# Kernel optimization log

Hardware: AMD Instinct MI355X
Metric: run time of the kernel (lower is better)

## Reference

```python
import jax, jax.numpy as jnp
import numpy as np

BATCH = 4        # opt.batch_size
NPATCH = 4096    # patches per batch element
DIM = 256        # feature dim
MAXC = 5         # self.max_classes
T = 0.07         # opt.nce_T
NEG_FILL = -10.0


def setup_inputs() -> dict:
    key = jax.random.key(0)
    k1, k2, k3 = jax.random.split(key, 3)
    N = BATCH * NPATCH
    features_src = jax.random.normal(k1, (N, DIM), jnp.float32)
    features_tgt = jax.random.normal(k2, (N, DIM), jnp.float32)
    classes = jax.random.randint(k3, (N,), 0, MAXC, dtype=jnp.int32)
    return {"features_src": features_src, "features_tgt": features_tgt, "classes": classes}


def reference(features_src, features_tgt, classes):
    # feat_k = feat_k.detach()
    tgt = jax.lax.stop_gradient(features_tgt)

    # positive logits: per-row dot product, divided by temperature
    pos = jnp.sum(features_src * tgt, axis=-1) / T            # [N]

    src_b = features_src.reshape(BATCH, NPATCH, DIM)
    tgt_b = tgt.reshape(BATCH, NPATCH, DIM)
    cls = classes.reshape(BATCH, NPATCH)

    # full negative logit matrix per batch element
    logits = jnp.einsum('bnd,bmd->bnm', src_b, tgt_b)         # [B, n, n]
    same = cls[:, :, None] == cls[:, None, :]                 # [B, n, n] same-class mask

    # per-class smallest negative logit: min over (row in class c, col not in class c)
    row_min = jnp.min(jnp.where(same, jnp.inf, logits), axis=2)          # [B, n]
    class_eq = cls[:, :, None] == jnp.arange(MAXC)[None, None, :]        # [B, n, C]
    class_min = jnp.min(jnp.where(class_eq, row_min[:, :, None], jnp.inf), axis=1)  # [B, C]
    smallest = jnp.minimum(class_min, NEG_FILL) / T                      # [B, C]
    counts = jnp.sum(class_eq, axis=1)                                   # [B, C]

    # per-row pad value and pad multiplicity (num_pairs_should - num_pairs_is = count_c - 1)
    sm_row = jnp.take_along_axis(smallest, cls, axis=1)                  # [B, n]
    npad = jnp.take_along_axis(counts, cls, axis=1) - 1                  # [B, n]

    # logsumexp over [pos, negatives (other classes only), npad copies of smallest]
    lse_neg = jax.nn.logsumexp(jnp.where(same, -jnp.inf, logits / T), axis=2)  # [B, n]
    pad_term = jnp.where(npad > 0,
                         jnp.log(jnp.maximum(npad, 1).astype(jnp.float32)) + sm_row,
                         -jnp.inf)
    pos_b = pos.reshape(BATCH, NPATCH)
    lse = jax.nn.logsumexp(jnp.stack([pos_b, lse_neg, pad_term], axis=-1), axis=-1)
    loss = lse - pos_b                                                   # CE with label 0

    # match torch ordering: rows concatenated per batch, grouped by class (stable)
    order = jnp.argsort(cls, axis=1)  # jnp.argsort is stable
    return jnp.take_along_axis(loss, order, axis=1).reshape(-1)
```

## Files before the change

kernel.cpp:

```cpp
#include <hip/hip_runtime.h>
#include <cstdint>

#define NBATCH 4
#define NPATCH 4096
#define MAXC   5
#define NCHUNK 8
#define RBLOCKS 16
#define GRID_MAIN (NBATCH * RBLOCKS * NCHUNK)
#define SCALE  14.285714285714286f
#define SCALE2 20.609929006188747f
#define LN2F   0.6931471805599453f
#define NEGH  -1.0e38f
#define NEGFILL_T -142.85714285714286f
#define NROWS (NBATCH * NPATCH)

typedef __attribute__((ext_vector_type(8))) short short8;
typedef __attribute__((ext_vector_type(4))) float f32x4;
typedef __attribute__((ext_vector_type(4))) unsigned int u32x4;

__device__ __forceinline__ float fexp2(float x) { return __builtin_amdgcn_exp2f(x); }
__device__ __forceinline__ float flog2(float x) { return __builtin_amdgcn_logf(x); }

__device__ __forceinline__ unsigned short f2bf(float f) {
  uint32_t u = __builtin_bit_cast(uint32_t, f);
  u = (u + 0x7FFFu + ((u >> 16) & 1u)) >> 16;
  return (unsigned short)u;
}

__device__ __forceinline__ void glds16(const void* g, void* l) {
  __builtin_amdgcn_global_load_lds(
      (const __attribute__((address_space(1))) uint32_t*)g,
      (__attribute__((address_space(3))) uint32_t*)l, 16, 0, 0);
}


__global__ __launch_bounds__(256) void k_aux(const float* __restrict__ src,
                                             const float* __restrict__ tgt,
                                             const int* __restrict__ classes,
                                             unsigned short* __restrict__ tgtb,
                                             unsigned short* __restrict__ srcb,
                                             float* __restrict__ pos,
                                             int* __restrict__ outpos,
                                             int* __restrict__ counts) {
  int blk = blockIdx.x;
  if (blk < 512) {
    __shared__ uint4 sS[2][544], sT[2][544];
    int t    = threadIdx.x;
    int half = t >> 7;
    int tt   = t & 127;
    int tl   = blk * 2 + half;
    int row16 = tt >> 3;
    int kg    = tt & 7;
    size_t rowbase = (size_t)(tl * 16 + row16) * 256 + kg * 32;
    const float4* rs  = (const float4*)(src + rowbase);
    const float4* rt_ = (const float4*)(tgt + rowbase);
    float d = 0.f;
#pragma unroll
    for (int jj = 0; jj < 4; ++jj) {
      float4 sa = rs[jj * 2], sb = rs[jj * 2 + 1];
      float4 ta = rt_[jj * 2], tb = rt_[jj * 2 + 1];
      d += sa.x * ta.x + sa.y * ta.y + sa.z * ta.z + sa.w * ta.w
         + sb.x * tb.x + sb.y * tb.y + sb.z * tb.z + sb.w * tb.w;
      union { ushort4 h[2]; uint4 u; } pk;
      int li = (kg * 4 + jj) * 17 + row16;
      pk.h[0].x = f2bf(sa.x * SCALE2); pk.h[0].y = f2bf(sa.y * SCALE2);
      pk.h[0].z = f2bf(sa.z * SCALE2); pk.h[0].w = f2bf(sa.w * SCALE2);
      pk.h[1].x = f2bf(sb.x * SCALE2); pk.h[1].y = f2bf(sb.y * SCALE2);
      pk.h[1].z = f2bf(sb.z * SCALE2); pk.h[1].w = f2bf(sb.w * SCALE2);
      sS[half][li] = pk.u;
      pk.h[0].x = f2bf(ta.x); pk.h[0].y = f2bf(ta.y);
      pk.h[0].z = f2bf(ta.z); pk.h[0].w = f2bf(ta.w);
      pk.h[1].x = f2bf(tb.x); pk.h[1].y = f2bf(tb.y);
      pk.h[1].z = f2bf(tb.z); pk.h[1].w = f2bf(tb.w);
      sT[half][li] = pk.u;
    }
    d += __shfl_xor(d, 1, 64);
    d += __shfl_xor(d, 2, 64);
    d += __shfl_xor(d, 4, 64);
    if (kg == 0) pos[tl * 16 + row16] = d * SCALE;

    __syncthreads();
    uint4* osrc = (uint4*)srcb + (size_t)tl * 512;
    uint4* otgt = (uint4*)tgtb + (size_t)tl * 512;
#pragma unroll
    for (int c = 0; c < 4; ++c) {
      int g  = c * 128 + tt;
      int li = (g >> 4) * 17 + (g & 15);
      osrc[g] = sS[half][li];
      otgt[g] = sT[half][li];
    }
    return;
  }

  __shared__ int sa[MAXC * 256];
  __shared__ int sb2[MAXC * 256];
  int b = blk - 512, t = threadIdx.x;
  int base = b * NPATCH + t * 16;
  int cv[16];
#pragma unroll
  for (int e = 0; e < 16; ++e) cv[e] = classes[base + e];
  int cnt[MAXC];
#pragma unroll
  for (int c = 0; c < MAXC; ++c) {
    cnt[c] = 0;
#pragma unroll
    for (int e = 0; e < 16; ++e)
      if (cv[e] == c) cnt[c]++;
  }
#pragma unroll
  for (int c = 0; c < MAXC; ++c) sa[c * 256 + t] = cnt[c];
  __syncthreads();

  int* rp = sa; int* wp = sb2;
  for (int d = 1; d < 256; d <<= 1) {
#pragma unroll
    for (int c = 0; c < MAXC; ++c) {
      int v = rp[c * 256 + t];
      if (t >= d) v += rp[c * 256 + t - d];
      wp[c * 256 + t] = v;
    }
    __syncthreads();
    int* tmp = rp; rp = wp; wp = tmp;
  }

  int tot[MAXC], excl[MAXC], off[MAXC + 1];
  off[0] = 0;
#pragma unroll
  for (int c = 0; c < MAXC; ++c) {
    tot[c]  = rp[c * 256 + 255];
    excl[c] = rp[c * 256 + t] - cnt[c];
    off[c + 1] = off[c] + tot[c];
  }
#pragma unroll
  for (int c = 0; c < MAXC; ++c) {
    int r = off[c] + excl[c];
#pragma unroll
    for (int e = 0; e < 16; ++e)
      if (cv[e] == c) { outpos[base + e] = r; r++; }
  }
  if (t < MAXC) counts[b * MAXC + t] = tot[t];
}

__global__ __launch_bounds__(256, 2) void k_main(const unsigned short* __restrict__ srcb,
                                                 const unsigned short* __restrict__ tgtb,
                                                 const int* __restrict__ classes,
                                                 float* __restrict__ pm,
                                                 float* __restrict__ ps) {
  __shared__ u32x4 sB[3][1024];

  const int p   = blockIdx.x;
  const int b   = p & 3;
  const int jl  = (p >> 2) & 1;
  const int rb  = (p >> 3) & 15;
  const int top = p >> 7;
  const int j   = top * 2 + jl;
  const int t0  = j * 16;
  const int nt  = 16;

  const int tid  = threadIdx.x;
  const int w    = tid >> 6;
  const int lane = tid & 63;
  const int q = lane >> 4, l4 = lane & 15;
  const int rowstart = b * NPATCH + rb * 256 + w * 64;

  const u32x4* ap = (const u32x4*)srcb + (size_t)(b * 256 + rb * 16 + w * 4) * 512 + lane;
  u32x4 afr[4][8];
#pragma unroll
  for (int rt = 0; rt < 4; ++rt)
#pragma unroll
    for (int ks = 0; ks < 8; ++ks)
      afr[rt][ks] = ap[rt * 512 + ks * 64];

  int rcls[4][4];
#pragma unroll
  for (int rt = 0; rt < 4; ++rt)
#pragma unroll
    for (int r = 0; r < 4; ++r)
      rcls[rt][r] = classes[rowstart + rt * 16 + q * 4 + r];

  float m_[4][4], s_[4][4];
#pragma unroll
  for (int rt = 0; rt < 4; ++rt)
#pragma unroll
    for (int r = 0; r < 4; ++r) { m_[rt][r] = -INFINITY; s_[rt][r] = 0.f; }

  const u32x4* bstage = (const u32x4*)tgtb + (size_t)(b * 256 + t0 * 2) * 512
                      + w * 64 + lane;
  const int* clp = classes + b * NPATCH + t0 * 32 + l4;

#define STAGE(NB, IT)                                                               \
  {                                                                                 \
    const u32x4* g = bstage + (size_t)(IT) * 1024;                                  \
    _Pragma("unroll")                                                               \
    for (int r = 0; r < 4; ++r)                                                     \
      glds16(g + r * 256, &sB[NB][(r * 4 + w) * 64]);                               \
  }

#define STATS(ac, cc0, cc1)                                                         \
  {                                                                                 \
    _Pragma("unroll")                                                               \
    for (int rt = 0; rt < 4; ++rt) {                                                \
      _Pragma("unroll")                                                             \
      for (int r = 0; r < 4; ++r) {                                                 \
        int rc = rcls[rt][r];                                                       \
        float y0 = ((cc0) == rc) ? NEGH : (ac)[rt][0][r];                           \
        float y1 = ((cc1) == rc) ? NEGH : (ac)[rt][1][r];                           \
        float nm = fmaxf(m_[rt][r], fmaxf(y0, y1));                                 \
        float e01 = fexp2(y0 - nm) + fexp2(y1 - nm);                                \
        s_[rt][r] = fmaf(s_[rt][r], fexp2(m_[rt][r] - nm), e01);                    \
        m_[rt][r] = nm;                                                             \
      }                                                                             \
    }                                                                               \
  }

  const f32x4 zc = {0.f, 0.f, 0.f, 0.f};

  STAGE(0, 0);
  STAGE(1, 1);
  asm volatile("s_waitcnt vmcnt(4)\n\ts_barrier" ::: "memory");

  for (int it = 0; it < nt; ++it) {
    const int cb = it % 3;
    const bool staged = (it + 2 < nt);
    if (staged) STAGE((it + 2) % 3, it + 2);

    int c0 = clp[0];
    int c1 = clp[16];
    clp += 32;

    f32x4 acc[4][2];
    {
      u32x4 e0[4], e1[4];
#pragma unroll
      for (int i = 0; i < 4; ++i) {
        e0[i] = sB[cb][i * 64 + lane];
        e1[i] = sB[cb][512 + i * 64 + lane];
      }
#pragma unroll
      for (int ksl = 0; ksl < 4; ++ksl) {
        short8 b0 = __builtin_bit_cast(short8, e0[ksl]);
        short8 b1 = __builtin_bit_cast(short8, e1[ksl]);
#pragma unroll
        for (int rt = 0; rt < 4; ++rt) {
          short8 a = __builtin_bit_cast(short8, afr[rt][ksl]);
          acc[rt][0] = __builtin_amdgcn_mfma_f32_16x16x32_bf16(
              a, b0, (ksl == 0) ? zc : acc[rt][0], 0, 0, 0);
          acc[rt][1] = __builtin_amdgcn_mfma_f32_16x16x32_bf16(
              a, b1, (ksl == 0) ? zc : acc[rt][1], 0, 0, 0);
        }
      }
    }
    {
      u32x4 e0[4], e1[4];
#pragma unroll
      for (int i = 0; i < 4; ++i) {
        e0[i] = sB[cb][256 + i * 64 + lane];
        e1[i] = sB[cb][768 + i * 64 + lane];
      }
#pragma unroll
      for (int ksl = 0; ksl < 4; ++ksl) {
        short8 b0 = __builtin_bit_cast(short8, e0[ksl]);
        short8 b1 = __builtin_bit_cast(short8, e1[ksl]);
#pragma unroll
        for (int rt = 0; rt < 4; ++rt) {
          short8 a = __builtin_bit_cast(short8, afr[rt][4 + ksl]);
          acc[rt][0] = __builtin_amdgcn_mfma_f32_16x16x32_bf16(a, b0, acc[rt][0], 0, 0, 0);
          acc[rt][1] = __builtin_amdgcn_mfma_f32_16x16x32_bf16(a, b1, acc[rt][1], 0, 0, 0);
        }
      }
    }

    STATS(acc, c0, c1);

    if (it + 1 < nt) {
      if (staged) asm volatile("s_waitcnt vmcnt(4)\n\ts_barrier" ::: "memory");
      else        asm volatile("s_waitcnt vmcnt(0)\n\ts_barrier" ::: "memory");
    }
  }
#undef STAGE
#undef STATS

#pragma unroll
  for (int off = 1; off < 16; off <<= 1) {
#pragma unroll
    for (int rt = 0; rt < 4; ++rt)
#pragma unroll
      for (int r = 0; r < 4; ++r) {
        float om = __shfl_xor(m_[rt][r], off, 64);
        float os = __shfl_xor(s_[rt][r], off, 64);
        float nm = fmaxf(m_[rt][r], om);
        s_[rt][r] = s_[rt][r] * fexp2(m_[rt][r] - nm) + os * fexp2(om - nm);
        m_[rt][r] = nm;
      }
  }

  if (l4 == 0) {
#pragma unroll
    for (int rt = 0; rt < 4; ++rt)
#pragma unroll
      for (int r = 0; r < 4; ++r) {
        size_t o = (size_t)j * NROWS + rowstart + rt * 16 + q * 4 + r;
        pm[o] = m_[rt][r];
        ps[o] = s_[rt][r];
      }
  }
}

__global__ __launch_bounds__(256) void k_fin(const int* __restrict__ classes,
                                             const float* __restrict__ pos,
                                             const float* __restrict__ pm,
                                             const float* __restrict__ ps,
                                             const int* __restrict__ outpos,
                                             const int* __restrict__ counts,
                                             float* __restrict__ out) {
  int n = blockIdx.x * 256 + threadIdx.x;
  int b = n >> 12;
  int c = classes[n];
  float ps_ = pos[n];

  float M2 = -INFINITY;
  float mm[NCHUNK], ss[NCHUNK];
#pragma unroll
  for (int s = 0; s < NCHUNK; ++s) {
    mm[s] = pm[(size_t)s * NROWS + n];
    ss[s] = ps[(size_t)s * NROWS + n];
    M2 = fmaxf(M2, mm[s]);
  }
  float S2 = 0.f;
#pragma unroll
  for (int s = 0; s < NCHUNK; ++s) S2 = fmaf(ss[s], fexp2(mm[s] - M2), S2);
  float ln = (S2 > 0.f) ? (M2 + flog2(S2)) * LN2F : -INFINITY;

  int npad = counts[b * MAXC + c] - 1;
  float pt = (npad > 0) ? (logf((float)npad) + NEGFILL_T) : -INFINITY;
  float M = fmaxf(ps_, fmaxf(ln, pt));
  float lse = M + logf(expf(ps_ - M) + expf(ln - M) + expf(pt - M));
  out[b * NPATCH + outpos[n]] = lse - ps_;
}

extern "C" void kernel_launch(void* const* d_in, const int* in_sizes, int n_in,
                              void* d_out, int out_size, void* d_ws, size_t ws_size,
                              hipStream_t stream) {
  const float* src = (const float*)d_in[0];
  const float* tgt = (const float*)d_in[1];
  const int* cls   = (const int*)d_in[2];
  float* out = (float*)d_out;

  char* ws = (char*)d_ws;
  unsigned short* tgtb = (unsigned short*)(ws);
  unsigned short* srcb = (unsigned short*)(ws + 8388608);
  float* pos    = (float*)(ws + 16777216);
  float* pm     = (float*)(ws + 16842752);
  float* ps     = (float*)(ws + 17367040);
  int*   outpos = (int*)  (ws + 17891328);
  int*   counts = (int*)  (ws + 17956864);

  k_aux<<<512 + NBATCH, 256, 0, stream>>>(src, tgt, cls, tgtb, srcb, pos, outpos, counts);
  k_main<<<GRID_MAIN, 256, 0, stream>>>(srcb, tgtb, cls, pm, ps);
  k_fin<<<NROWS / 256, 256, 0, stream>>>(cls, pos, pm, ps, outpos, counts, out);
}
```

Before: 128.3 us.

## Use 8 waves per block in main kernel with fewer row tiles per wave

The main kernel now runs 512 threads per block, each wave handling 32 rows instead of 64. This halves the per-wave A fragments and accumulators, which cuts register pressure and raises the occupancy target to 4. Staging of B into LDS is split across 8 waves with two loads each, and the B fragments are now read from LDS one step at a time instead of being preloaded. The finalize kernel moves to 64-thread blocks. The cost is more waves sharing each LDS tile, so more LDS reads per MFMA and less reuse of each B fragment.

```diff
diff --git a/kernel.cpp b/kernel.cpp
--- a/kernel.cpp
+++ b/kernel.cpp
@@ -141,7 +141,7 @@
   if (t < MAXC) counts[b * MAXC + t] = tot[t];
 }
 
-__global__ __launch_bounds__(256, 2) void k_main(const unsigned short* __restrict__ srcb,
+__global__ __launch_bounds__(512, 4) void k_main(const unsigned short* __restrict__ srcb,
                                                  const unsigned short* __restrict__ tgtb,
                                                  const int* __restrict__ classes,
                                                  float* __restrict__ pm,
@@ -161,26 +161,26 @@
   const int w    = tid >> 6;
   const int lane = tid & 63;
   const int q = lane >> 4, l4 = lane & 15;
-  const int rowstart = b * NPATCH + rb * 256 + w * 64;
-
-  const u32x4* ap = (const u32x4*)srcb + (size_t)(b * 256 + rb * 16 + w * 4) * 512 + lane;
-  u32x4 afr[4][8];
-#pragma unroll
-  for (int rt = 0; rt < 4; ++rt)
+  const int rowstart = b * NPATCH + rb * 256 + w * 32;
+
+  const u32x4* ap = (const u32x4*)srcb + (size_t)(b * 256 + rb * 16 + w * 2) * 512 + lane;
+  u32x4 afr[2][8];
+#pragma unroll
+  for (int rt = 0; rt < 2; ++rt)
 #pragma unroll
     for (int ks = 0; ks < 8; ++ks)
       afr[rt][ks] = ap[rt * 512 + ks * 64];
 
-  int rcls[4][4];
-#pragma unroll
-  for (int rt = 0; rt < 4; ++rt)
+  int rcls[2][4];
+#pragma unroll
+  for (int rt = 0; rt < 2; ++rt)
 #pragma unroll
     for (int r = 0; r < 4; ++r)
       rcls[rt][r] = classes[rowstart + rt * 16 + q * 4 + r];
 
-  float m_[4][4], s_[4][4];
-#pragma unroll
-  for (int rt = 0; rt < 4; ++rt)
+  float m_[2][4], s_[2][4];
+#pragma unroll
+  for (int rt = 0; rt < 2; ++rt)
 #pragma unroll
     for (int r = 0; r < 4; ++r) { m_[rt][r] = -INFINITY; s_[rt][r] = 0.f; }
 
@@ -191,15 +191,14 @@
 #define STAGE(NB, IT)                                                               \
   {                                                                                 \
     const u32x4* g = bstage + (size_t)(IT) * 1024;                                  \
-    _Pragma("unroll")                                                               \
-    for (int r = 0; r < 4; ++r)                                                     \
-      glds16(g + r * 256, &sB[NB][(r * 4 + w) * 64]);                               \
+    glds16(g,       &sB[NB][w * 64]);                                               \
+    glds16(g + 512, &sB[NB][(8 + w) * 64]);                                         \
   }
 
 #define STATS(ac, cc0, cc1)                                                         \
   {                                                                                 \
     _Pragma("unroll")                                                               \
-    for (int rt = 0; rt < 4; ++rt) {                                                \
+    for (int rt = 0; rt < 2; ++rt) {                                                \
       _Pragma("unroll")                                                             \
       for (int r = 0; r < 4; ++r) {                                                 \
         int rc = rcls[rt][r];                                                       \
@@ -217,7 +216,7 @@
 
   STAGE(0, 0);
   STAGE(1, 1);
-  asm volatile("s_waitcnt vmcnt(4)\n\ts_barrier" ::: "memory");
+  asm volatile("s_waitcnt vmcnt(2)\n\ts_barrier" ::: "memory");
 
   for (int it = 0; it < nt; ++it) {
     const int cb = it % 3;
@@ -228,52 +227,40 @@
     int c1 = clp[16];
     clp += 32;
 
-    f32x4 acc[4][2];
-    {
-      u32x4 e0[4], e1[4];
-#pragma unroll
-      for (int i = 0; i < 4; ++i) {
-        e0[i] = sB[cb][i * 64 + lane];
-        e1[i] = sB[cb][512 + i * 64 + lane];
+    f32x4 acc[2][2];
+#pragma unroll
+    for (int ksl = 0; ksl < 4; ++ksl) {
+      u32x4 e0 = sB[cb][ksl * 64 + lane];
+      u32x4 e1 = sB[cb][512 + ksl * 64 + lane];
+      short8 b0 = __builtin_bit_cast(short8, e0);
+      short8 b1 = __builtin_bit_cast(short8, e1);
+#pragma unroll
+      for (int rt = 0; rt < 2; ++rt) {
+        short8 a = __builtin_bit_cast(short8, afr[rt][ksl]);
+        acc[rt][0] = __builtin_amdgcn_mfma_f32_16x16x32_bf16(
+            a, b0, (ksl == 0) ? zc : acc[rt][0], 0, 0, 0);
+        acc[rt][1] = __builtin_amdgcn_mfma_f32_16x16x32_bf16(
+            a, b1, (ksl == 0) ? zc : acc[rt][1], 0, 0, 0);
       }
-#pragma unroll
-      for (int ksl = 0; ksl < 4; ++ksl) {
-        short8 b0 = __builtin_bit_cast(short8, e0[ksl]);
-        short8 b1 = __builtin_bit_cast(short8, e1[ksl]);
-#pragma unroll
-        for (int rt = 0; rt < 4; ++rt) {
-          short8 a = __builtin_bit_cast(short8, afr[rt][ksl]);
-          acc[rt][0] = __builtin_amdgcn_mfma_f32_16x16x32_bf16(
-              a, b0, (ksl == 0) ? zc : acc[rt][0], 0, 0, 0);
-          acc[rt][1] = __builtin_amdgcn_mfma_f32_16x16x32_bf16(
-              a, b1, (ksl == 0) ? zc : acc[rt][1], 0, 0, 0);
-        }
+    }
+#pragma unroll
+    for (int ksl = 0; ksl < 4; ++ksl) {
+      u32x4 e0 = sB[cb][256 + ksl * 64 + lane];
+      u32x4 e1 = sB[cb][768 + ksl * 64 + lane];
+      short8 b0 = __builtin_bit_cast(short8, e0);
+      short8 b1 = __builtin_bit_cast(short8, e1);
+#pragma unroll
+      for (int rt = 0; rt < 2; ++rt) {
+        short8 a = __builtin_bit_cast(short8, afr[rt][4 + ksl]);
+        acc[rt][0] = __builtin_amdgcn_mfma_f32_16x16x32_bf16(a, b0, acc[rt][0], 0, 0, 0);
+        acc[rt][1] = __builtin_amdgcn_mfma_f32_16x16x32_bf16(a, b1, acc[rt][1], 0, 0, 0);
       }
     }
-    {
-      u32x4 e0[4], e1[4];
-#pragma unroll
-      for (int i = 0; i < 4; ++i) {
-        e0[i] = sB[cb][256 + i * 64 + lane];
-        e1[i] = sB[cb][768 + i * 64 + lane];
-      }
-#pragma unroll
-      for (int ksl = 0; ksl < 4; ++ksl) {
-        short8 b0 = __builtin_bit_cast(short8, e0[ksl]);
-        short8 b1 = __builtin_bit_cast(short8, e1[ksl]);
-#pragma unroll
-        for (int rt = 0; rt < 4; ++rt) {
-          short8 a = __builtin_bit_cast(short8, afr[rt][4 + ksl]);
-          acc[rt][0] = __builtin_amdgcn_mfma_f32_16x16x32_bf16(a, b0, acc[rt][0], 0, 0, 0);
-          acc[rt][1] = __builtin_amdgcn_mfma_f32_16x16x32_bf16(a, b1, acc[rt][1], 0, 0, 0);
-        }
-      }
-    }
 
     STATS(acc, c0, c1);
 
     if (it + 1 < nt) {
-      if (staged) asm volatile("s_waitcnt vmcnt(4)\n\ts_barrier" ::: "memory");
+      if (staged) asm volatile("s_waitcnt vmcnt(2)\n\ts_barrier" ::: "memory");
       else        asm volatile("s_waitcnt vmcnt(0)\n\ts_barrier" ::: "memory");
     }
   }
@@ -283,7 +270,7 @@
 #pragma unroll
   for (int off = 1; off < 16; off <<= 1) {
 #pragma unroll
-    for (int rt = 0; rt < 4; ++rt)
+    for (int rt = 0; rt < 2; ++rt)
 #pragma unroll
       for (int r = 0; r < 4; ++r) {
         float om = __shfl_xor(m_[rt][r], off, 64);
@@ -296,7 +283,7 @@
 
   if (l4 == 0) {
 #pragma unroll
-    for (int rt = 0; rt < 4; ++rt)
+    for (int rt = 0; rt < 2; ++rt)
 #pragma unroll
       for (int r = 0; r < 4; ++r) {
         size_t o = (size_t)j * NROWS + rowstart + rt * 16 + q * 4 + r;
@@ -306,14 +293,14 @@
   }
 }
 
-__global__ __launch_bounds__(256) void k_fin(const int* __restrict__ classes,
-                                             const float* __restrict__ pos,
-                                             const float* __restrict__ pm,
-                                             const float* __restrict__ ps,
-                                             const int* __restrict__ outpos,
-                                             const int* __restrict__ counts,
-                                             float* __restrict__ out) {
-  int n = blockIdx.x * 256 + threadIdx.x;
+__global__ __launch_bounds__(64) void k_fin(const int* __restrict__ classes,
+                                            const float* __restrict__ pos,
+                                            const float* __restrict__ pm,
+                                            const float* __restrict__ ps,
+                                            const int* __restrict__ outpos,
+                                            const int* __restrict__ counts,
+                                            float* __restrict__ out) {
+  int n = blockIdx.x * 64 + threadIdx.x;
   int b = n >> 12;
   int c = classes[n];
   float ps_ = pos[n];
@@ -356,6 +343,6 @@
   int*   counts = (int*)  (ws + 17956864);
 
   k_aux<<<512 + NBATCH, 256, 0, stream>>>(src, tgt, cls, tgtb, srcb, pos, outpos, counts);
-  k_main<<<GRID_MAIN, 256, 0, stream>>>(srcb, tgtb, cls, pm, ps);
-  k_fin<<<NROWS / 256, 256, 0, stream>>>(cls, pos, pm, ps, outpos, counts, out);
-}
+  k_main<<<GRID_MAIN, 512, 0, stream>>>(srcb, tgtb, cls, pm, ps);
+  k_fin<<<NROWS / 64, 64, 0, stream>>>(cls, pos, pm, ps, outpos, counts, out);
+}
```

After: 124.6 us. -2.9%, faster.
